# Kernel optimization log

Hardware: AMD Instinct MI355X
Metric: run time of the kernel (lower is better)

Reference implementation:

```python
import jax, jax.numpy as jnp
import numpy as np

N_NODES = 100000
N_EDGES = 1600000
N_GRAPHS = 256
D = 128
L = 3
N_OUT = 10


def setup_inputs() -> dict:
    key = jax.random.key(0)
    ks = jax.random.split(key, 6)
    x = jax.random.normal(ks[0], (N_NODES, D), dtype=jnp.float32)
    edge_index = jax.random.randint(ks[1], (2, N_EDGES), 0, N_NODES, dtype=jnp.int64)
    batch = jnp.sort(jax.random.randint(ks[2], (N_NODES,), 0, N_GRAPHS, dtype=jnp.int64))
    conv_w = jax.random.normal(ks[3], (L, D, D), dtype=jnp.float32) * (1.0 / np.sqrt(D))
    conv_b = jnp.zeros((L, D), dtype=jnp.float32)
    out_w = jax.random.normal(ks[4], (3 * D, N_OUT), dtype=jnp.float32) * (1.0 / np.sqrt(3 * D))
    out_b = jnp.zeros((N_OUT,), dtype=jnp.float32)
    return {"x": x, "edge_index": edge_index, "batch": batch,
            "conv_w": conv_w, "conv_b": conv_b, "out_w": out_w, "out_b": out_b}


def reference(x, edge_index, batch, conv_w, conv_b, out_w, out_b):
    N = x.shape[0]
    # --- add self-loops (PyG GCNConv default) ---
    loop = jnp.arange(N, dtype=edge_index.dtype)
    src = jnp.concatenate([edge_index[0], loop])  # [E+N]
    dst = jnp.concatenate([edge_index[1], loop])
    # --- symmetric normalization: deg computed on dst (col) ---
    deg = jax.ops.segment_sum(jnp.ones_like(dst, dtype=x.dtype), dst, num_segments=N)
    dinv = jnp.where(deg > 0, jax.lax.rsqrt(jnp.maximum(deg, 1.0)), 0.0)
    norm = dinv[src] * dinv[dst]  # [E+N]

    h = x
    for l in range(conv_w.shape[0]):
        h = h @ conv_w[l]                                   # [N, D] transform first
        msg = h[src] * norm[:, None]                        # gather + scale
        h = jax.ops.segment_sum(msg, dst, num_segments=N)   # scatter-add
        h = jax.nn.relu(h + conv_b[l])

    # --- global max / mean / add pooling over graphs ---
    B = N_GRAPHS
    gmax = jax.ops.segment_max(h, batch, num_segments=B)
    gsum = jax.ops.segment_sum(h, batch, num_segments=B)
    cnt = jax.ops.segment_sum(jnp.ones((N, 1), h.dtype), batch, num_segments=B)
    gmean = gsum / jnp.maximum(cnt, 1.0)
    pooled = jnp.concatenate([gmax, gmean, gsum], axis=1)   # [B, 3D]
    # dropout p=0.5 is identity in eval mode
    return pooled @ out_w + out_b
```

## Files before the change

kernel.cpp:

```cpp
#include <hip/hip_runtime.h>
#include <hip/hip_bf16.h>

#define D 128
#define NP 8
#define DPB 64
#define KPB (DPB * NP)
#define SUB 64
#define CAP_SUB 64

typedef __attribute__((ext_vector_type(8))) __bf16 bf16x8;
typedef __attribute__((ext_vector_type(4))) float f32x4;
typedef __attribute__((ext_vector_type(4))) short s16x4;
typedef __attribute__((ext_vector_type(8))) short s16x8;

static __device__ __forceinline__ short f2bf(float f) {
    union { float f; unsigned u; } in; in.f = f;
    unsigned u = in.u;
    u += 0x7fffu + ((u >> 16) & 1u);
    return (short)(u >> 16);
}

__global__ void k_bucket(const int* __restrict__ src, const int* __restrict__ dst,
                         int* __restrict__ bcnt, int* __restrict__ staging,
                         int E, int KBE) {
    int i = blockIdx.x * 256 + threadIdx.x;
    if (i >= E) return;
    int d = dst[i], s = src[i];
    int b = d >> 6;
    int key = ((d & 63) << 3) | (s >> 14);
    int j = blockIdx.x & (SUB - 1);
    int slot = atomicAdd(&bcnt[j * KBE + b], 1);
    if (slot < CAP_SUB) staging[((size_t)j * KBE + b) * CAP_SUB + slot] = (key << 17) | s;
}

__global__ void k_btot(const int* __restrict__ bcnt, int* __restrict__ btot, int KBE) {
    int b = blockIdx.x * 256 + threadIdx.x;
    if (b >= KBE) return;
    int v = 0;
    #pragma unroll
    for (int j = 0; j < SUB; j++) {
        int c = bcnt[j * KBE + b];
        v += (c > CAP_SUB) ? CAP_SUB : c;
    }
    btot[b] = v;
}

__global__ void k_bscan(const int* __restrict__ btot, int* __restrict__ bbase,
                        int* __restrict__ row_ptr, int nkeys, int KBE) {
    __shared__ int sm[512];
    __shared__ int carry;
    int t = threadIdx.x;
    if (t == 0) carry = 0;
    __syncthreads();
    for (int c0 = 0; c0 < KBE; c0 += 512) {
        int b = c0 + t;
        int v = (b < KBE) ? btot[b] : 0;
        sm[t] = v;
        __syncthreads();
        for (int off = 1; off < 512; off <<= 1) {
            int x = (t >= off) ? sm[t - off] : 0;
            __syncthreads();
            sm[t] += x;
            __syncthreads();
        }
        if (b < KBE) bbase[b] = sm[t] - v + carry;
        __syncthreads();
        if (t == 0) carry += sm[511];
        __syncthreads();
    }
    if (t == 0) { bbase[KBE] = carry; row_ptr[nkeys] = carry; }
}

__global__ __launch_bounds__(256) void k_build(
    const int* __restrict__ staging, const int* __restrict__ bcnt,
    const int* __restrict__ bbase, int* __restrict__ row_ptr,
    int* __restrict__ csr_src, float* __restrict__ dinv, int N, int KBE)
{
    const int b = blockIdx.x;
    const int tid = threadIdx.x;
    __shared__ int cnt[KPB];
    __shared__ int subn[SUB];
    __shared__ int chunkbuf[256];
    __shared__ int carry;

    if (tid < SUB) {
        int c = bcnt[tid * KBE + b];
        subn[tid] = (c > CAP_SUB) ? CAP_SUB : c;
    }
    for (int k = tid; k < KPB; k += 256) cnt[k] = 0;
    if (tid == 0) carry = 0;
    __syncthreads();

    const int base = bbase[b];
    const int nb = bbase[b + 1] - base;
    const int j = tid >> 2, l4 = tid & 3;
    const int* __restrict__ sreg = staging + ((size_t)j * KBE + b) * CAP_SUB;
    const int sn = subn[j];

    for (int e = l4; e < sn; e += 4)
        atomicAdd(&cnt[sreg[e] >> 17], 1);
    __syncthreads();

    #pragma unroll 1
    for (int c = 0; c < KPB / 256; c++) {
        int idx = c * 256 + tid;
        int v = cnt[idx];
        chunkbuf[tid] = v;
        __syncthreads();
        for (int off = 1; off < 256; off <<= 1) {
            int x = (tid >= off) ? chunkbuf[tid - off] : 0;
            __syncthreads();
            chunkbuf[tid] += x;
            __syncthreads();
        }
        cnt[idx] = chunkbuf[tid] - v + carry;
        __syncthreads();
        if (tid == 255) carry += chunkbuf[255];
        __syncthreads();
    }

    for (int k = tid; k < KPB; k += 256)
        row_ptr[(size_t)b * KPB + k] = base + cnt[k];
    for (int dl = tid; dl < DPB; dl += 256) {
        int d = b * DPB + dl;
        if (d < N) {
            int hi2 = (dl == DPB - 1) ? nb : cnt[(dl + 1) * NP];
            int deg = hi2 - cnt[dl * NP];
            dinv[d] = rsqrtf((float)deg + 1.0f);
        }
    }
    __syncthreads();

    for (int e = l4; e < sn; e += 4) {
        int w = sreg[e];
        int slot = base + atomicAdd(&cnt[w >> 17], 1);
        csr_src[slot] = w & 0x1FFFF;
    }
}

__global__ void k_gseg(const int* __restrict__ batch, int* __restrict__ gstart,
                       int* __restrict__ gcnt, int N, int B) {
    int g = blockIdx.x * blockDim.x + threadIdx.x;
    if (g > B) return;
    int lo = 0, hi = N;
    while (lo < hi) {
        int mid = (lo + hi) >> 1;
        if (batch[mid] < g) lo = mid + 1; else hi = mid;
    }
    gstart[g] = lo;
    if (g < B) {
        int lo2 = lo, hi2 = N;
        while (lo2 < hi2) {
            int mid = (lo2 + hi2) >> 1;
            if (batch[mid] < g + 1) lo2 = mid + 1; else hi2 = mid;
        }
        gcnt[g] = lo2 - lo;
    }
}

__global__ void k_cvt_x(const float* __restrict__ x, const float* __restrict__ dinv,
                        short* __restrict__ xb, int total4) {
    int i = blockIdx.x * blockDim.x + threadIdx.x;
    if (i < total4) {
        float d = dinv[i >> 5];
        float4 v = ((const float4*)x)[i];
        s16x4 o;
        o.x = f2bf(v.x * d); o.y = f2bf(v.y * d);
        o.z = f2bf(v.z * d); o.w = f2bf(v.w * d);
        ((s16x4*)xb)[i] = o;
    }
}

__global__ void k_cvt_w(const float* __restrict__ W, short* __restrict__ Wt, int total) {
    int i = blockIdx.x * blockDim.x + threadIdx.x;
    if (i < total) {
        int l = i >> 14;
        int rem = i & 16383;
        int n = rem >> 7;
        int k = rem & 127;
        Wt[i] = f2bf(W[(l << 14) + (k << 7) + n]);
    }
}

__global__ __launch_bounds__(256) void k_layer(
    const short* __restrict__ hin, const int* __restrict__ row_ptr,
    const int* __restrict__ csr_src, const float* __restrict__ dinv,
    const short* __restrict__ Wt, const float* __restrict__ bias,
    short* __restrict__ hout, float* __restrict__ hrelu, int N, int mode)
{
    __shared__ __align__(16) short tile[16 * 128];
    const int tid = threadIdx.x;
    const int wave = tid >> 6;
    const int lane = tid & 63;
    const int group = lane >> 4;
    const int lg = lane & 15;
    const int off = lg * 8;
    const int node_base = blockIdx.x * 16;
    const int r = wave * 4 + group;
    const int i = node_base + r;

    short* dstp = &tile[r * 128 + ((lg ^ (r & 7)) << 3)];
    if (i < N) {
        float acc[8];
        bf16x8 v = *(const bf16x8*)(hin + (size_t)i * D + off);
        #pragma unroll
        for (int k = 0; k < 8; k++) acc[k] = (float)v[k];
        const int kb = i * NP;
        int s = row_ptr[kb];
        #pragma unroll 1
        for (int p = 0; p < NP; p++) {
            int e = row_ptr[kb + p + 1];
            for (int t = s; t < e; t += 4) {
                int i0 = csr_src[t];
                int i1 = (t + 1 < e) ? csr_src[t + 1] : -1;
                int i2 = (t + 2 < e) ? csr_src[t + 2] : -1;
                int i3 = (t + 3 < e) ? csr_src[t + 3] : -1;
                bf16x8 v0 = *(const bf16x8*)(hin + (size_t)i0 * D + off);
                bf16x8 v1, v2, v3;
                if (i1 >= 0) v1 = *(const bf16x8*)(hin + (size_t)i1 * D + off);
                if (i2 >= 0) v2 = *(const bf16x8*)(hin + (size_t)i2 * D + off);
                if (i3 >= 0) v3 = *(const bf16x8*)(hin + (size_t)i3 * D + off);
                #pragma unroll
                for (int k = 0; k < 8; k++) acc[k] += (float)v0[k];
                if (i1 >= 0) {
                    #pragma unroll
                    for (int k = 0; k < 8; k++) acc[k] += (float)v1[k];
                }
                if (i2 >= 0) {
                    #pragma unroll
                    for (int k = 0; k < 8; k++) acc[k] += (float)v2[k];
                }
                if (i3 >= 0) {
                    #pragma unroll
                    for (int k = 0; k < 8; k++) acc[k] += (float)v3[k];
                }
            }
            s = e;
        }
        const float di = dinv[i];
        s16x8 o;
        #pragma unroll
        for (int k = 0; k < 8; k++) o[k] = f2bf(acc[k] * di);
        *(s16x8*)dstp = o;
    } else {
        s16x8 z = {0, 0, 0, 0, 0, 0, 0, 0};
        *(s16x8*)dstp = z;
    }
    __syncthreads();

    bf16x8 afrag[4];
    #pragma unroll
    for (int kt = 0; kt < 4; kt++)
        afrag[kt] = *(const bf16x8*)(&tile[lg * 128 + (((group + 4 * kt) ^ (lg & 7)) << 3)]);

    f32x4 acc2[2];
    #pragma unroll
    for (int nt = 0; nt < 2; nt++) { f32x4 z = {0.f, 0.f, 0.f, 0.f}; acc2[nt] = z; }
    #pragma unroll
    for (int nt = 0; nt < 2; nt++) {
        const short* bp = Wt + (size_t)(wave * 32 + nt * 16 + lg) * D + group * 8;
        #pragma unroll
        for (int kt = 0; kt < 4; kt++) {
            bf16x8 b = *(const bf16x8*)(bp + kt * 32);
            acc2[nt] = __builtin_amdgcn_mfma_f32_16x16x32_bf16(afrag[kt], b, acc2[nt], 0, 0, 0);
        }
    }

    float bcol[2];
    #pragma unroll
    for (int nt = 0; nt < 2; nt++) bcol[nt] = bias[wave * 32 + nt * 16 + lg];
    const int row0 = node_base + group * 4;
    #pragma unroll
    for (int i2 = 0; i2 < 4; i2++) {
        int r2 = row0 + i2;
        if (r2 < N) {
            if (mode == 0) {
                float dr = dinv[r2];
                #pragma unroll
                for (int nt = 0; nt < 2; nt++) {
                    int col = wave * 32 + nt * 16 + lg;
                    float val = fmaxf(acc2[nt][i2] + bcol[nt], 0.0f);
                    hout[(size_t)r2 * D + col] = f2bf(val * dr);
                }
            } else {
                #pragma unroll
                for (int nt = 0; nt < 2; nt++) {
                    int col = wave * 32 + nt * 16 + lg;
                    hrelu[(size_t)r2 * D + col] = fmaxf(acc2[nt][i2] + bcol[nt], 0.0f);
                }
            }
        }
    }
}

__global__ __launch_bounds__(256) void k_pool(const float* __restrict__ hrelu,
                                              const int* __restrict__ gstart,
                                              const int* __restrict__ gcnt,
                                              float* __restrict__ pmax,
                                              float* __restrict__ psum, int B) {
    int g = blockIdx.x >> 2;
    int q = blockIdx.x & 3;
    int c = threadIdx.x & 127;
    int p = threadIdx.x >> 7;
    int start = gstart[g];
    int endr = start + gcnt[g];

    float mx0 = 0.f, mx1 = 0.f, sm0 = 0.f, sm1 = 0.f;
    int r = start + q * 2 + p;
    for (; r + 8 < endr; r += 16) {
        float v0 = hrelu[(size_t)r * D + c];
        float v1 = hrelu[(size_t)(r + 8) * D + c];
        mx0 = fmaxf(mx0, v0); sm0 += v0;
        mx1 = fmaxf(mx1, v1); sm1 += v1;
    }
    if (r < endr) {
        float v0 = hrelu[(size_t)r * D + c];
        mx0 = fmaxf(mx0, v0); sm0 += v0;
    }
    float mx = fmaxf(mx0, mx1), sm = sm0 + sm1;

    __shared__ float smx[128], ssm[128];
    if (p == 1) { smx[c] = mx; ssm[c] = sm; }
    __syncthreads();
    if (p == 0) {
        pmax[((size_t)q * B + g) * D + c] = fmaxf(mx, smx[c]);
        psum[((size_t)q * B + g) * D + c] = sm + ssm[c];
    }
}

__global__ void k_final(const float* __restrict__ pmax, const float* __restrict__ psum,
                        const int* __restrict__ gcnt, const float* __restrict__ ow,
                        const float* __restrict__ ob, float* __restrict__ out, int B) {
    int g = blockIdx.x;
    int t = threadIdx.x;
    float part[10];
    #pragma unroll
    for (int o = 0; o < 10; o++) part[o] = 0.f;
    float invc = 1.0f / fmaxf((float)gcnt[g], 1.0f);
    for (int k = t; k < 3 * D; k += 64) {
        int c = (k < D) ? k : ((k < 2 * D) ? k - D : k - 2 * D);
        float pk;
        if (k < D) {
            float m = pmax[(size_t)g * D + c];
            #pragma unroll
            for (int q = 1; q < 4; q++) m = fmaxf(m, pmax[((size_t)q * B + g) * D + c]);
            pk = m;
        } else {
            float s = psum[(size_t)g * D + c];
            #pragma unroll
            for (int q = 1; q < 4; q++) s += psum[((size_t)q * B + g) * D + c];
            pk = (k < 2 * D) ? s * invc : s;
        }
        const float* w = ow + k * 10;
        #pragma unroll
        for (int o = 0; o < 10; o++) part[o] += pk * w[o];
    }
    #pragma unroll
    for (int off = 32; off > 0; off >>= 1)
        #pragma unroll
        for (int o = 0; o < 10; o++) part[o] += __shfl_down(part[o], off, 64);
    if (t == 0)
        #pragma unroll
        for (int o = 0; o < 10; o++) out[g * 10 + o] = part[o] + ob[o];
}

extern "C" void kernel_launch(void* const* d_in, const int* in_sizes, int n_in,
                              void* d_out, int out_size, void* d_ws, size_t ws_size,
                              hipStream_t stream) {
    const float* x     = (const float*)d_in[0];
    const int*   ei    = (const int*)d_in[1];
    const int*   batch = (const int*)d_in[2];
    const float* convw = (const float*)d_in[3];
    const float* convb = (const float*)d_in[4];
    const float* outw  = (const float*)d_in[5];
    const float* outb  = (const float*)d_in[6];
    float* out = (float*)d_out;

    const int N = in_sizes[0] / D;
    const int E = in_sizes[1] / 2;
    const int L = in_sizes[3] / (D * D);
    const int B = out_size / 10;

    const int* src = ei;
    const int* dst = ei + E;

    const int KBE   = (N + DPB - 1) / DPB;
    const int nkeys = KBE * KPB;

    char* p = (char*)d_ws;
    auto alloc = [&](size_t bytes) { char* r = p; p += (bytes + 255) & ~255ull; return r; };
    short* hb0     = (short*)alloc((size_t)N * D * 2);
    short* hb1     = (short*)alloc((size_t)N * D * 2);
    float* hrelu   = (float*)alloc((size_t)N * D * 4);
    short* Wt      = (short*)alloc((size_t)L * D * D * 2);
    int*   row_ptr = (int*)alloc(((size_t)nkeys + 1) * 4);
    int*   csr_src = (int*)alloc((size_t)E * 4);
    int*   bcnt    = (int*)alloc((size_t)SUB * KBE * 4);
    int*   btot    = (int*)alloc((size_t)KBE * 4);
    int*   bbase   = (int*)alloc(((size_t)KBE + 1) * 4);
    float* dinv    = (float*)alloc((size_t)N * 4);
    float* pmax    = (float*)alloc((size_t)4 * B * D * 4);
    float* psum    = (float*)alloc((size_t)4 * B * D * 4);
    int*   gcnt    = (int*)alloc((size_t)B * 4);
    int*   gstart  = (int*)alloc(((size_t)B + 1) * 4);

    int* staging = (int*)hrelu;

    hipMemsetAsync(bcnt, 0, (size_t)SUB * KBE * 4, stream);

    k_bucket<<<(E + 255) / 256, 256, 0, stream>>>(src, dst, bcnt, staging, E, KBE);
    k_gseg<<<1, 512, 0, stream>>>(batch, gstart, gcnt, N, B);
    k_btot<<<(KBE + 255) / 256, 256, 0, stream>>>(bcnt, btot, KBE);
    k_bscan<<<1, 512, 0, stream>>>(btot, bbase, row_ptr, nkeys, KBE);
    k_build<<<KBE, 256, 0, stream>>>(staging, bcnt, bbase, row_ptr, csr_src, dinv, N, KBE);
    k_cvt_x<<<((N * D / 4) + 255) / 256, 256, 0, stream>>>(x, dinv, hb0, N * D / 4);
    k_cvt_w<<<((L * D * D) + 255) / 256, 256, 0, stream>>>(convw, Wt, L * D * D);

    const int lblocks = (N + 15) / 16;
    k_layer<<<lblocks, 256, 0, stream>>>(hb0, row_ptr, csr_src, dinv, Wt,
                                         convb, hb1, hrelu, N, 0);
    k_layer<<<lblocks, 256, 0, stream>>>(hb1, row_ptr, csr_src, dinv, Wt + D * D,
                                         convb + D, hb0, hrelu, N, 0);
    k_layer<<<lblocks, 256, 0, stream>>>(hb0, row_ptr, csr_src, dinv, Wt + 2 * D * D,
                                         convb + 2 * D, hb1, hrelu, N, 1);

    k_pool<<<B * 4, 256, 0, stream>>>(hrelu, gstart, gcnt, pmax, psum, B);
    k_final<<<B, 64, 0, stream>>>(pmax, psum, gcnt, outw, outb, out, B);
}
```

Baseline: 469.6 us.

## Sort nodes by degree within buckets and unroll neighbor gather by eight

After: 497.1 us. +5.8%, slower.

```diff
diff --git a/kernel.cpp b/kernel.cpp
--- a/kernel.cpp
+++ b/kernel.cpp
@@ -74,12 +74,14 @@
 __global__ __launch_bounds__(256) void k_build(
     const int* __restrict__ staging, const int* __restrict__ bcnt,
     const int* __restrict__ bbase, int* __restrict__ row_ptr,
-    int* __restrict__ csr_src, float* __restrict__ dinv, int N, int KBE)
+    int* __restrict__ csr_src, float* __restrict__ dinv,
+    int* __restrict__ perm, int N, int KBE)
 {
     const int b = blockIdx.x;
     const int tid = threadIdx.x;
     __shared__ int cnt[KPB];
     __shared__ int subn[SUB];
+    __shared__ int sdeg[DPB];
     __shared__ int chunkbuf[256];
     __shared__ int carry;
 
@@ -121,12 +123,16 @@
 
     for (int k = tid; k < KPB; k += 256)
         row_ptr[(size_t)b * KPB + k] = base + cnt[k];
-    for (int dl = tid; dl < DPB; dl += 256) {
+    if (tid < DPB) {
+        int dl = tid;
         int d = b * DPB + dl;
+        int hi2 = (dl == DPB - 1) ? nb : cnt[(dl + 1) * NP];
+        int deg = hi2 - cnt[dl * NP];
         if (d < N) {
-            int hi2 = (dl == DPB - 1) ? nb : cnt[(dl + 1) * NP];
-            int deg = hi2 - cnt[dl * NP];
             dinv[d] = rsqrtf((float)deg + 1.0f);
+            sdeg[dl] = deg;
+        } else {
+            sdeg[dl] = 0x7FFFFFFF;
         }
     }
     __syncthreads();
@@ -135,6 +141,17 @@
         int w = sreg[e];
         int slot = base + atomicAdd(&cnt[w >> 17], 1);
         csr_src[slot] = w & 0x1FFFF;
+    }
+
+    if (tid < DPB) {
+        int mydeg = sdeg[tid];
+        int rank = 0;
+        #pragma unroll
+        for (int q = 0; q < DPB; q++) {
+            int dq = sdeg[q];
+            rank += (dq < mydeg) || (dq == mydeg && q < tid);
+        }
+        perm[b * DPB + rank] = b * DPB + tid;
     }
 }
 
@@ -185,10 +202,12 @@
 __global__ __launch_bounds__(256) void k_layer(
     const short* __restrict__ hin, const int* __restrict__ row_ptr,
     const int* __restrict__ csr_src, const float* __restrict__ dinv,
-    const short* __restrict__ Wt, const float* __restrict__ bias,
-    short* __restrict__ hout, float* __restrict__ hrelu, int N, int mode)
+    const int* __restrict__ perm, const short* __restrict__ Wt,
+    const float* __restrict__ bias, short* __restrict__ hout,
+    float* __restrict__ hrelu, int N, int mode)
 {
     __shared__ __align__(16) short tile[16 * 128];
+    __shared__ int snode[16];
     const int tid = threadIdx.x;
     const int wave = tid >> 6;
     const int lane = tid & 63;
@@ -197,7 +216,8 @@
     const int off = lg * 8;
     const int node_base = blockIdx.x * 16;
     const int r = wave * 4 + group;
-    const int i = node_base + r;
+    const int i = perm[node_base + r];
+    if (lg == 0) snode[r] = i;
 
     short* dstp = &tile[r * 128 + ((lg ^ (r & 7)) << 3)];
     if (i < N) {
@@ -205,38 +225,46 @@
         bf16x8 v = *(const bf16x8*)(hin + (size_t)i * D + off);
         #pragma unroll
         for (int k = 0; k < 8; k++) acc[k] = (float)v[k];
-        const int kb = i * NP;
-        int s = row_ptr[kb];
-        #pragma unroll 1
-        for (int p = 0; p < NP; p++) {
-            int e = row_ptr[kb + p + 1];
-            for (int t = s; t < e; t += 4) {
-                int i0 = csr_src[t];
-                int i1 = (t + 1 < e) ? csr_src[t + 1] : -1;
-                int i2 = (t + 2 < e) ? csr_src[t + 2] : -1;
-                int i3 = (t + 3 < e) ? csr_src[t + 3] : -1;
-                bf16x8 v0 = *(const bf16x8*)(hin + (size_t)i0 * D + off);
-                bf16x8 v1, v2, v3;
-                if (i1 >= 0) v1 = *(const bf16x8*)(hin + (size_t)i1 * D + off);
-                if (i2 >= 0) v2 = *(const bf16x8*)(hin + (size_t)i2 * D + off);
-                if (i3 >= 0) v3 = *(const bf16x8*)(hin + (size_t)i3 * D + off);
-                #pragma unroll
-                for (int k = 0; k < 8; k++) acc[k] += (float)v0[k];
-                if (i1 >= 0) {
-                    #pragma unroll
-                    for (int k = 0; k < 8; k++) acc[k] += (float)v1[k];
-                }
-                if (i2 >= 0) {
-                    #pragma unroll
-                    for (int k = 0; k < 8; k++) acc[k] += (float)v2[k];
-                }
-                if (i3 >= 0) {
-                    #pragma unroll
-                    for (int k = 0; k < 8; k++) acc[k] += (float)v3[k];
-                }
-            }
-            s = e;
-        }
+        int t = row_ptr[i * NP];
+        const int end = row_ptr[i * NP + NP];
+
+        for (; t + 8 <= end; t += 8) {
+            int i0 = csr_src[t + 0], i1 = csr_src[t + 1];
+            int i2 = csr_src[t + 2], i3 = csr_src[t + 3];
+            int i4 = csr_src[t + 4], i5 = csr_src[t + 5];
+            int i6 = csr_src[t + 6], i7 = csr_src[t + 7];
+            bf16x8 v0 = *(const bf16x8*)(hin + (size_t)i0 * D + off);
+            bf16x8 v1 = *(const bf16x8*)(hin + (size_t)i1 * D + off);
+            bf16x8 v2 = *(const bf16x8*)(hin + (size_t)i2 * D + off);
+            bf16x8 v3 = *(const bf16x8*)(hin + (size_t)i3 * D + off);
+            bf16x8 v4 = *(const bf16x8*)(hin + (size_t)i4 * D + off);
+            bf16x8 v5 = *(const bf16x8*)(hin + (size_t)i5 * D + off);
+            bf16x8 v6 = *(const bf16x8*)(hin + (size_t)i6 * D + off);
+            bf16x8 v7 = *(const bf16x8*)(hin + (size_t)i7 * D + off);
+            #pragma unroll
+            for (int k = 0; k < 8; k++)
+                acc[k] += (((float)v0[k] + (float)v1[k]) + ((float)v2[k] + (float)v3[k]))
+                        + (((float)v4[k] + (float)v5[k]) + ((float)v6[k] + (float)v7[k]));
+        }
+        if (t + 4 <= end) {
+            int i0 = csr_src[t + 0], i1 = csr_src[t + 1];
+            int i2 = csr_src[t + 2], i3 = csr_src[t + 3];
+            bf16x8 v0 = *(const bf16x8*)(hin + (size_t)i0 * D + off);
+            bf16x8 v1 = *(const bf16x8*)(hin + (size_t)i1 * D + off);
+            bf16x8 v2 = *(const bf16x8*)(hin + (size_t)i2 * D + off);
+            bf16x8 v3 = *(const bf16x8*)(hin + (size_t)i3 * D + off);
+            #pragma unroll
+            for (int k = 0; k < 8; k++)
+                acc[k] += (((float)v0[k] + (float)v1[k]) + ((float)v2[k] + (float)v3[k]));
+            t += 4;
+        }
+        for (; t < end; t++) {
+            int i0 = csr_src[t];
+            bf16x8 v0 = *(const bf16x8*)(hin + (size_t)i0 * D + off);
+            #pragma unroll
+            for (int k = 0; k < 8; k++) acc[k] += (float)v0[k];
+        }
+
         const float di = dinv[i];
         s16x8 o;
         #pragma unroll
@@ -269,10 +297,9 @@
     float bcol[2];
     #pragma unroll
     for (int nt = 0; nt < 2; nt++) bcol[nt] = bias[wave * 32 + nt * 16 + lg];
-    const int row0 = node_base + group * 4;
     #pragma unroll
     for (int i2 = 0; i2 < 4; i2++) {
-        int r2 = row0 + i2;
+        int r2 = snode[group * 4 + i2];
         if (r2 < N) {
             if (mode == 0) {
                 float dr = dinv[r2];
@@ -398,6 +425,7 @@
     int*   bcnt    = (int*)alloc((size_t)SUB * KBE * 4);
     int*   btot    = (int*)alloc((size_t)KBE * 4);
     int*   bbase   = (int*)alloc(((size_t)KBE + 1) * 4);
+    int*   perm    = (int*)alloc((size_t)KBE * DPB * 4);
     float* dinv    = (float*)alloc((size_t)N * 4);
     float* pmax    = (float*)alloc((size_t)4 * B * D * 4);
     float* psum    = (float*)alloc((size_t)4 * B * D * 4);
@@ -412,16 +440,16 @@
     k_gseg<<<1, 512, 0, stream>>>(batch, gstart, gcnt, N, B);
     k_btot<<<(KBE + 255) / 256, 256, 0, stream>>>(bcnt, btot, KBE);
     k_bscan<<<1, 512, 0, stream>>>(btot, bbase, row_ptr, nkeys, KBE);
-    k_build<<<KBE, 256, 0, stream>>>(staging, bcnt, bbase, row_ptr, csr_src, dinv, N, KBE);
+    k_build<<<KBE, 256, 0, stream>>>(staging, bcnt, bbase, row_ptr, csr_src, dinv, perm, N, KBE);
     k_cvt_x<<<((N * D / 4) + 255) / 256, 256, 0, stream>>>(x, dinv, hb0, N * D / 4);
     k_cvt_w<<<((L * D * D) + 255) / 256, 256, 0, stream>>>(convw, Wt, L * D * D);
 
     const int lblocks = (N + 15) / 16;
-    k_layer<<<lblocks, 256, 0, stream>>>(hb0, row_ptr, csr_src, dinv, Wt,
+    k_layer<<<lblocks, 256, 0, stream>>>(hb0, row_ptr, csr_src, dinv, perm, Wt,
                                          convb, hb1, hrelu, N, 0);
-    k_layer<<<lblocks, 256, 0, stream>>>(hb1, row_ptr, csr_src, dinv, Wt + D * D,
+    k_layer<<<lblocks, 256, 0, stream>>>(hb1, row_ptr, csr_src, dinv, perm, Wt + D * D,
                                          convb + D, hb0, hrelu, N, 0);
-    k_layer<<<lblocks, 256, 0, stream>>>(hb0, row_ptr, csr_src, dinv, Wt + 2 * D * D,
+    k_layer<<<lblocks, 256, 0, stream>>>(hb0, row_ptr, csr_src, dinv, perm, Wt + 2 * D * D,
                                          convb + 2 * D, hb1, hrelu, N, 1);
 
     k_pool<<<B * 4, 256, 0, stream>>>(hrelu, gstart, gcnt, pmax, psum, B);
```
